# Optimization experiments

Hardware: AMD Instinct MI355X
Metric: run time of the kernel (lower is better)

Reference implementation:

```python
import jax, jax.numpy as jnp
import numpy as np

B, S, HID, H, RELC = 2, 1024, 1024, 16, 64
D = HID // H          # head dim = 64
R = 2 * RELC + 1      # 129 relative-position buckets
NEG_INF = -10000.0
LN_EPS = 1e-12


def setup_inputs() -> dict:
    key = jax.random.key(0)
    ks = jax.random.split(key, 16)
    s = 0.02
    return {
        "query": jax.random.normal(ks[0], (B, S, HID), jnp.float32),
        "key": jax.random.normal(ks[1], (B, S, HID), jnp.float32),
        "value": jax.random.normal(ks[2], (B, S, HID), jnp.float32),
        "mask_k": jnp.ones((B, S), jnp.float32),
        "mask_qk": jnp.ones((B, S, S), jnp.float32),
        "rposi": jax.random.randint(ks[3], (B, S, S), 0, R, jnp.int32),
        "Wq": jax.random.normal(ks[4], (HID, HID), jnp.float32) * s,
        "bq": jnp.zeros((HID,), jnp.float32),
        "Wk": jax.random.normal(ks[5], (HID, HID), jnp.float32) * s,
        "bk": jnp.zeros((HID,), jnp.float32),
        "Wv": jax.random.normal(ks[6], (HID, HID), jnp.float32) * s,
        "bv": jnp.zeros((HID,), jnp.float32),
        "Wd": jax.random.normal(ks[7], (HID, HID), jnp.float32) * s,
        "bd": jnp.zeros((HID,), jnp.float32),
        "ln_g": jnp.ones((HID,), jnp.float32),
        "ln_b": jnp.zeros((HID,), jnp.float32),
        "edge_atts": jax.random.normal(ks[8], (R, D), jnp.float32) * s,
        "edge_values": jax.random.normal(ks[9], (R, D), jnp.float32) * s,
    }


def _heads(x):  # [B,S,HID] -> [B,H,S,D]
    return x.reshape(B, -1, H, D).transpose(0, 2, 1, 3)


def reference(query, key, value, mask_k, mask_qk, rposi,
              Wq, bq, Wk, bk, Wv, bv, Wd, bd, ln_g, ln_b,
              edge_atts, edge_values):
    q = _heads(query @ Wq + bq)   # [B,H,Q,D]
    k = _heads(key @ Wk + bk)     # [B,H,K,D]
    v = _heads(value @ Wv + bv)   # [B,H,K,D]

    rp = jnp.clip(rposi, -RELC, RELC) + RELC          # [B,Q,K] in [0,2*RELC]

    scores = jnp.einsum('bhqd,bhkd->bhqk', q, k)      # [B,H,Q,K]
    # relative-position attention bias: q . edge_atts[rp]
    q2 = jnp.einsum('bhqd,rd->bhqr', q, edge_atts)    # [B,H,Q,R]
    rscore = jnp.take_along_axis(
        q2, jnp.broadcast_to(rp[:, None], (B, H, S, S)), axis=-1)
    scores = (scores + rscore) / jnp.sqrt(jnp.float32(D))

    att_mask = mask_k[:, None, :] * mask_qk           # [B,Q,K]
    scores = scores + (1.0 - att_mask)[:, None] * NEG_INF
    probs = jax.nn.softmax(scores, axis=-1)           # [B,H,Q,K]

    ctx = jnp.einsum('bhqk,bhkd->bhqd', probs, v)     # [B,H,Q,D]
    rval = edge_values[rp]                            # [B,Q,K,D]
    ctx = ctx + jnp.einsum('bhqk,bqkd->bhqd', probs, rval)

    ctx = ctx.transpose(0, 2, 1, 3).reshape(B, S, HID)
    h = ctx @ Wd + bd
    x = h + query
    mu = jnp.mean(x, axis=-1, keepdims=True)
    var = jnp.mean(jnp.square(x - mu), axis=-1, keepdims=True)
    return (x - mu) * jax.lax.rsqrt(var + LN_EPS) * ln_g + ln_b
```

## Files before the change

### kernel.cpp

```cpp
#include <hip/hip_runtime.h>
#include <hip/hip_bf16.h>
#include <stdint.h>

#define B_    2
#define S_    1024
#define HID_  1024
#define H_    16
#define D_    64
#define R_    129
#define EST_  136
#define SENT_ 132
#define NTOK_ 2048
#define C2_   0.18033688011112042f

typedef __attribute__((ext_vector_type(8))) short bf16x8;
typedef __attribute__((ext_vector_type(4))) float f32x4;

__device__ __forceinline__ float bf2f(unsigned short s) {
  union { float f; unsigned int u; } v; v.u = ((unsigned int)s) << 16; return v.f;
}
__device__ __forceinline__ unsigned short f2bf(float f) {
  union { float f; unsigned int u; } v; v.f = f;
  return (unsigned short)((v.u + 0x7fff + ((v.u >> 16) & 1)) >> 16);
}

__global__ __launch_bounds__(256) void wt4_kernel(const float* __restrict__ Wq,
                                                  const float* __restrict__ Wk,
                                                  const float* __restrict__ Wv,
                                                  const float* __restrict__ Wd,
                                                  unsigned short* __restrict__ WqT,
                                                  unsigned short* __restrict__ WkT,
                                                  unsigned short* __restrict__ WvT,
                                                  unsigned short* __restrict__ WdT) {
  const float* W; unsigned short* Wt;
  switch (blockIdx.z) {
    case 0: W = Wq; Wt = WqT; break;
    case 1: W = Wk; Wt = WkT; break;
    case 2: W = Wv; Wt = WvT; break;
    default: W = Wd; Wt = WdT; break;
  }
  __shared__ float tile[32][33];
  const int n0 = blockIdx.x * 32, k0 = blockIdx.y * 32;
  const int tx = threadIdx.x, ty = threadIdx.y;
  #pragma unroll
  for (int i = 0; i < 32; i += 8)
    tile[ty + i][tx] = W[(size_t)(k0 + ty + i) * HID_ + n0 + tx];
  __syncthreads();
  #pragma unroll
  for (int i = 0; i < 32; i += 8)
    Wt[(size_t)(n0 + ty + i) * HID_ + k0 + tx] = f2bf(tile[tx][ty + i]);
}

__global__ __launch_bounds__(256) void evt_kernel(const float* __restrict__ EV,
                                                  unsigned short* __restrict__ EVt) {
  const int idx = blockIdx.x * 256 + threadIdx.x;
  if (idx < 64 * 160) {
    const int d = idx / 160, r = idx % 160;
    EVt[idx] = f2bf(r < R_ ? EV[(size_t)r * D_ + d] : 0.f);
  }
}

__global__ __launch_bounds__(256) void rpx_kernel(const int* __restrict__ rposi,
                                                  const float* __restrict__ mask_k,
                                                  const float* __restrict__ mask_qk,
                                                  unsigned char* __restrict__ rpx) {
  const int t = threadIdx.x;
  const int lo = t & 15, hi = (t >> 4) & 3, wq = (t >> 6) & 1, wk = (t >> 7) & 1;
  const int kt = blockIdx.x, q5 = blockIdx.y, b = blockIdx.z;
  unsigned char out[8];
  #pragma unroll
  for (int e = 0; e < 8; e++) {
    const int ct2 = e >> 2, j = e & 3;
    const int q = q5 * 32 + wq * 16 + hi * 4 + j;
    const int k = kt * 64 + wk * 32 + ct2 * 16 + lo;
    int rp = rposi[((size_t)b * S_ + q) * S_ + k];
    rp = min(max(rp, -64), 64) + 64;
    const float m = mask_qk[((size_t)b * S_ + q) * S_ + k] * mask_k[(size_t)b * S_ + k];
    out[e] = (m > 0.5f) ? (unsigned char)rp : (unsigned char)SENT_;
  }
  const size_t off = ((((((size_t)b * 32 + q5) * 16 + kt) * 2 + wk) * 2 + wq) * 4 + hi) * 16 + lo;
  *(uint2*)(rpx + off * 8) = *(uint2*)out;
}

__global__ __launch_bounds__(256) void qkv_gemm_kernel(
    const float* __restrict__ query, const float* __restrict__ key, const float* __restrict__ value,
    const unsigned short* __restrict__ WqT, const unsigned short* __restrict__ WkT,
    const unsigned short* __restrict__ WvT,
    const float* __restrict__ bq, const float* __restrict__ bk, const float* __restrict__ bvv,
    unsigned short* __restrict__ Qh, unsigned short* __restrict__ Kh, unsigned short* __restrict__ Vt) {
  const float* A; const unsigned short* Bt; const float* bias; unsigned short* Out; int omode;
  if (blockIdx.z == 0)      { A = query; Bt = WqT; bias = bq;  Out = Qh; omode = 0; }
  else if (blockIdx.z == 1) { A = key;   Bt = WkT; bias = bk;  Out = Kh; omode = 0; }
  else                      { A = value; Bt = WvT; bias = bvv; Out = Vt; omode = 1; }
  __shared__ __align__(16) unsigned short Alds[64][40];
  __shared__ __align__(16) unsigned short Blds[128][40];
  const int m0 = blockIdx.x * 64, n0 = blockIdx.y * 128;
  const int t = threadIdx.x;
  const int wave = t >> 6, lane = t & 63, lo = lane & 15, hi = lane >> 4;
  const int wr = wave >> 1, wc = wave & 1;
  const int arow = t >> 2, acol = (t & 3) * 8;
  const int brow = t >> 1, bcol = (t & 1) * 16;
  const f32x4 zero4 = {0.f, 0.f, 0.f, 0.f};
  f32x4 acc[2][4];
  #pragma unroll
  for (int a = 0; a < 2; a++)
    #pragma unroll
    for (int b = 0; b < 4; b++) acc[a][b] = zero4;

  for (int k0 = 0; k0 < HID_; k0 += 32) {
    const float* asrc = A + (size_t)(m0 + arow) * HID_ + k0 + acol;
    f32x4 v0 = *(const f32x4*)asrc, v1 = *(const f32x4*)(asrc + 4);
    unsigned short ab[8];
    ab[0]=f2bf(v0.x); ab[1]=f2bf(v0.y); ab[2]=f2bf(v0.z); ab[3]=f2bf(v0.w);
    ab[4]=f2bf(v1.x); ab[5]=f2bf(v1.y); ab[6]=f2bf(v1.z); ab[7]=f2bf(v1.w);
    bf16x8 bb0 = *(const bf16x8*)(Bt + (size_t)(n0 + brow) * HID_ + k0 + bcol);
    bf16x8 bb1 = *(const bf16x8*)(Bt + (size_t)(n0 + brow) * HID_ + k0 + bcol + 8);
    __syncthreads();
    *(bf16x8*)&Alds[arow][acol]     = *(bf16x8*)ab;
    *(bf16x8*)&Blds[brow][bcol]     = bb0;
    *(bf16x8*)&Blds[brow][bcol + 8] = bb1;
    __syncthreads();
    bf16x8 af[2], bfr[4];
    #pragma unroll
    for (int a = 0; a < 2; a++) af[a]  = *(const bf16x8*)&Alds[wr*32 + a*16 + lo][hi*8];
    #pragma unroll
    for (int b = 0; b < 4; b++) bfr[b] = *(const bf16x8*)&Blds[wc*64 + b*16 + lo][hi*8];
    #pragma unroll
    for (int a = 0; a < 2; a++)
      #pragma unroll
      for (int b = 0; b < 4; b++)
        acc[a][b] = __builtin_amdgcn_mfma_f32_16x16x32_bf16(af[a], bfr[b], acc[a][b], 0, 0, 0);
  }

  #pragma unroll
  for (int a = 0; a < 2; a++) {
    const int mg = m0 + wr*32 + a*16 + hi*4;
    #pragma unroll
    for (int b = 0; b < 4; b++) {
      const int n = n0 + wc*64 + b*16 + lo;
      const float bv = bias[n];
      const int hh = n >> 6, d = n & (D_ - 1);
      #pragma unroll
      for (int j = 0; j < 4; j++) {
        const float val = acc[a][b][j] + bv;
        const int m = mg + j;
        const int bb = m >> 10, s = m & (S_ - 1);
        if (omode == 0)
          Out[(((size_t)(bb * H_ + hh)) * S_ + s) * D_ + d] = f2bf(val);
        else
          Out[(((size_t)(bb * H_ + hh)) * D_ + d) * S_ + s] = f2bf(val);
      }
    }
  }
}

__global__ __launch_bounds__(256) void d_gemm_kernel(const unsigned short* __restrict__ Actx,
                                                     const unsigned short* __restrict__ Bt,
                                                     const float* __restrict__ bias,
                                                     float* __restrict__ Out) {
  __shared__ __align__(16) unsigned short Alds[64][40];
  __shared__ __align__(16) unsigned short Blds[128][40];
  const int m0 = blockIdx.x * 64, n0 = blockIdx.y * 128;
  const int t = threadIdx.x;
  const int wave = t >> 6, lane = t & 63, lo = lane & 15, hi = lane >> 4;
  const int wr = wave >> 1, wc = wave & 1;
  const int arow = t >> 2, acol = (t & 3) * 8;
  const int brow = t >> 1, bcol = (t & 1) * 16;
  const f32x4 zero4 = {0.f, 0.f, 0.f, 0.f};
  f32x4 acc[2][4];
  #pragma unroll
  for (int a = 0; a < 2; a++)
    #pragma unroll
    for (int b = 0; b < 4; b++) acc[a][b] = zero4;

  for (int k0 = 0; k0 < HID_; k0 += 32) {
    bf16x8 aa = *(const bf16x8*)(Actx + (size_t)(m0 + arow) * HID_ + k0 + acol);
    bf16x8 bb0 = *(const bf16x8*)(Bt + (size_t)(n0 + brow) * HID_ + k0 + bcol);
    bf16x8 bb1 = *(const bf16x8*)(Bt + (size_t)(n0 + brow) * HID_ + k0 + bcol + 8);
    __syncthreads();
    *(bf16x8*)&Alds[arow][acol]     = aa;
    *(bf16x8*)&Blds[brow][bcol]     = bb0;
    *(bf16x8*)&Blds[brow][bcol + 8] = bb1;
    __syncthreads();
    bf16x8 af[2], bfr[4];
    #pragma unroll
    for (int a = 0; a < 2; a++) af[a]  = *(const bf16x8*)&Alds[wr*32 + a*16 + lo][hi*8];
    #pragma unroll
    for (int b = 0; b < 4; b++) bfr[b] = *(const bf16x8*)&Blds[wc*64 + b*16 + lo][hi*8];
    #pragma unroll
    for (int a = 0; a < 2; a++)
      #pragma unroll
      for (int b = 0; b < 4; b++)
        acc[a][b] = __builtin_amdgcn_mfma_f32_16x16x32_bf16(af[a], bfr[b], acc[a][b], 0, 0, 0);
  }

  #pragma unroll
  for (int a = 0; a < 2; a++) {
    const int mg = m0 + wr*32 + a*16 + hi*4;
    #pragma unroll
    for (int b = 0; b < 4; b++) {
      const int n = n0 + wc*64 + b*16 + lo;
      const float bv = bias[n];
      #pragma unroll
      for (int j = 0; j < 4; j++)
        Out[(size_t)(mg + j) * HID_ + n] = acc[a][b][j] + bv;
    }
  }
}

__global__ __launch_bounds__(256) void eb_kernel(const unsigned short* __restrict__ Qh,
                                                 const float* __restrict__ EA,
                                                 unsigned short* __restrict__ Eb) {
  __shared__ __align__(16) unsigned short Qt[64][72];
  __shared__ __align__(16) unsigned short EAt[144][72];
  const int bh = blockIdx.y, s0 = blockIdx.x * 64;
  const int t = threadIdx.x, wave = t >> 6, lane = t & 63;
  const int lo = lane & 15, hi = lane >> 4;
  { const int row = t >> 2, c0 = (t & 3) * 16;
    const unsigned short* src = Qh + ((size_t)bh * S_ + s0 + row) * D_ + c0;
    *(bf16x8*)&Qt[row][c0]   = *(const bf16x8*)src;
    *(bf16x8*)&Qt[row][c0+8] = *(const bf16x8*)(src + 8); }
  for (int i = t; i < 144 * 64; i += 256) {
    const int r = i >> 6, d = i & 63;
    EAt[r][d] = f2bf(r < R_ ? EA[(size_t)r * D_ + d] : 0.f);
  }
  __syncthreads();
  bf16x8 af[2];
  af[0] = *(const bf16x8*)&Qt[wave*16 + lo][hi*8];
  af[1] = *(const bf16x8*)&Qt[wave*16 + lo][32 + hi*8];
  const f32x4 zero4 = {0.f, 0.f, 0.f, 0.f};
  f32x4 acc[9];
  #pragma unroll
  for (int rt = 0; rt < 9; rt++) acc[rt] = zero4;
  #pragma unroll
  for (int rt = 0; rt < 9; rt++)
    #pragma unroll
    for (int kk = 0; kk < 2; kk++) {
      bf16x8 bfr = *(const bf16x8*)&EAt[rt*16 + lo][kk*32 + hi*8];
      acc[rt] = __builtin_amdgcn_mfma_f32_16x16x32_bf16(af[kk], bfr, acc[rt], 0, 0, 0);
    }
  #pragma unroll
  for (int rt = 0; rt < 9; rt++) {
    const int r = rt * 16 + lo;
    if (r < EST_) {
      #pragma unroll
      for (int j = 0; j < 4; j++) {
        const int q = s0 + wave*16 + hi*4 + j;
        const float val = (r < R_) ? exp2f(acc[rt][j] * C2_) : 0.f;
        Eb[((size_t)bh * S_ + q) * EST_ + r] = f2bf(val);
      }
    }
  }
}


#define ABODY(KT, RX) do {                                                               \
    const int kw = (KT) * 64 + wk * 32;                                                  \
    float ge[8];                                                                         \
    _Pragma("unroll")                                                                    \
    for (int e = 0; e < 8; e++) {                                                        \
      const int rp = (int)(((e < 4 ? (RX).x : (RX).y) >> ((e & 3) * 8)) & 255u);         \
      ge[e] = bf2f(Uq.El[wq * 16 + hi * 4 + (e & 3)][rp]);                               \
    }                                                                                    \
    bf16x8 kf0 = *(const bf16x8*)(Kbase + (size_t)(kw + lo) * D_ + hi * 8);              \
    bf16x8 kf1 = *(const bf16x8*)(Kbase + (size_t)(kw + lo) * D_ + 32 + hi * 8);         \
    bf16x8 kf2 = *(const bf16x8*)(Kbase + (size_t)(kw + 16 + lo) * D_ + hi * 8);         \
    bf16x8 kf3 = *(const bf16x8*)(Kbase + (size_t)(kw + 16 + lo) * D_ + 32 + hi * 8);    \
    bf16x8 vf0 = *(const bf16x8*)(Vbase + (size_t)(lo) * S_ + kw + hi * 8);              \
    bf16x8 vf1 = *(const bf16x8*)(Vbase + (size_t)(16 + lo) * S_ + kw + hi * 8);         \
    bf16x8 vf2 = *(const bf16x8*)(Vbase + (size_t)(32 + lo) * S_ + kw + hi * 8);         \
    bf16x8 vf3 = *(const bf16x8*)(Vbase + (size_t)(48 + lo) * S_ + kw + hi * 8);         \
    f32x4 sc0 = zero4, sc1 = zero4;                                                      \
    sc0 = __builtin_amdgcn_mfma_f32_16x16x32_bf16(qfrag0, kf0, sc0, 0, 0, 0);            \
    sc0 = __builtin_amdgcn_mfma_f32_16x16x32_bf16(qfrag1, kf1, sc0, 0, 0, 0);            \
    sc1 = __builtin_amdgcn_mfma_f32_16x16x32_bf16(qfrag0, kf2, sc1, 0, 0, 0);            \
    sc1 = __builtin_amdgcn_mfma_f32_16x16x32_bf16(qfrag1, kf3, sc1, 0, 0, 0);            \
    unsigned int pvp0, pvp1, pvp2, pvp3;                                                 \
    _Pragma("unroll")                                                                    \
    for (int e = 0; e < 8; e++) {                                                        \
      const int j = e & 3;                                                               \
      const float sv = (e < 4) ? sc0[j] : sc1[j];                                        \
      const float p = exp2f(sv * C2_) * ge[e];                                           \
      lsum[j] += p;                                                                      \
      const unsigned int pb = f2bf(p);                                                   \
      if (e == 0) pvp0 = pb;       else if (e == 1) pvp0 |= pb << 16;                    \
      else if (e == 2) pvp1 = pb;  else if (e == 3) pvp1 |= pb << 16;                    \
      else if (e == 4) pvp2 = pb;  else if (e == 5) pvp2 |= pb << 16;                    \
      else if (e == 6) pvp3 = pb;  else              pvp3 |= pb << 16;                   \
      Plds[wave][hi * 4 + j][(e >> 2) * 16 + lo] = (unsigned short)pb;                   \
    }                                                                                    \
    bf16x8 pf = *(const bf16x8*)&Plds[wave][lo][hi * 8];                                 \
    ctx[0] = __builtin_amdgcn_mfma_f32_16x16x32_bf16(pf, vf0, ctx[0], 0, 0, 0);          \
    ctx[1] = __builtin_amdgcn_mfma_f32_16x16x32_bf16(pf, vf1, ctx[1], 0, 0, 0);          \
    ctx[2] = __builtin_amdgcn_mfma_f32_16x16x32_bf16(pf, vf2, ctx[2], 0, 0, 0);          \
    ctx[3] = __builtin_amdgcn_mfma_f32_16x16x32_bf16(pf, vf3, ctx[3], 0, 0, 0);          \
    _Pragma("unroll")                                                                    \
    for (int e = 0; e < 8; e++) {                                                        \
      const int rp = (int)(((e < 4 ? (RX).x : (RX).y) >> ((e & 3) * 8)) & 255u);         \
      const unsigned int pw = (e < 2) ? pvp0 : (e < 4) ? pvp1 : (e < 6) ? pvp2 : pvp3;   \
      const float pr = bf2f((unsigned short)((pw >> ((e & 1) * 16)) & 0xFFFFu));         \
      if (rp == 128) r128[e & 3] += pr;                                                  \
      else atomicAdd(&hist[wq * 16 + hi * 4 + (e & 3)][rp], pr);                         \
    }                                                                                    \
  } while (0)

__global__ __launch_bounds__(256, 4) void attn_kernel(const unsigned short* __restrict__ Qh,
                                                      const unsigned short* __restrict__ Kh,
                                                      const unsigned short* __restrict__ Vt,
                                                      const unsigned short* __restrict__ Eb,
                                                      const unsigned char* __restrict__ rpx,
                                                      const unsigned short* __restrict__ EVt,
                                                      unsigned short* __restrict__ ctxb) {
  __shared__ union UU {
    unsigned short El[32][EST_];
    float red[2][16][65];
  } Uq;
  __shared__ float hist[32][EST_];
  __shared__ __align__(16) unsigned short Plds[4][16][40];
  __shared__ float lsumLDS[2][32];

  const int lin = blockIdx.x;
  const int bh = (lin & 7) + 8 * (lin >> 8);
  const int q5 = (lin >> 3) & 31;
  const int b = bh >> 4, h = bh & 15;
  const int q0 = q5 * 32;
  const int t = threadIdx.x, wave = t >> 6, lane = t & 63;
  const int lo = lane & 15, hi = lane >> 4;
  const int wq = wave >> 1, wk = wave & 1;

  { const unsigned int* src = (const unsigned int*)(Eb + ((size_t)bh * S_ + q0) * EST_);
    unsigned int* dst = (unsigned int*)&Uq.El[0][0];
    for (int i = t; i < 32 * EST_ / 2; i += 256) dst[i] = src[i]; }
  for (int i = t; i < 32 * EST_; i += 256) (&hist[0][0])[i] = 0.f;

  bf16x8 qfrag0, qfrag1;
  { const unsigned short* qrow = Qh + ((size_t)bh * S_ + q0 + wq * 16 + lo) * D_;
    qfrag0 = *(const bf16x8*)(qrow + hi * 8);
    qfrag1 = *(const bf16x8*)(qrow + 32 + hi * 8); }

  const f32x4 zero4 = {0.f, 0.f, 0.f, 0.f};
  f32x4 ctx[4] = {zero4, zero4, zero4, zero4};
  float lsum[4] = {0.f, 0.f, 0.f, 0.f};
  float r128[4] = {0.f, 0.f, 0.f, 0.f};

  const unsigned short* Kbase = Kh + (size_t)bh * S_ * D_;
  const unsigned short* Vbase = Vt + (size_t)bh * D_ * S_;
  const unsigned char* RXp = rpx +
      (((((((size_t)b * 32 + q5) * 16) * 2 + wk) * 2 + wq) * 4 + hi) * 16 + lo) * 8;

  __syncthreads();

  uint2 rxA = *(const uint2*)(RXp);
  #pragma unroll 1
  for (int kt2 = 0; kt2 < 8; kt2++) {
    uint2 rxB = *(const uint2*)(RXp + (size_t)(2 * kt2 + 1) * 2048);
    ABODY(2 * kt2, rxA);
    if (kt2 < 7) rxA = *(const uint2*)(RXp + (size_t)(2 * kt2 + 2) * 2048);
    ABODY(2 * kt2 + 1, rxB);
  }

  #pragma unroll
  for (int j = 0; j < 4; j++) {
    float v = r128[j];
    v += __shfl_xor(v, 1); v += __shfl_xor(v, 2); v += __shfl_xor(v, 4); v += __shfl_xor(v, 8);
    if (lo == 0) atomicAdd(&hist[wq * 16 + hi * 4 + j][128], v);
    float w = lsum[j];
    w += __shfl_xor(w, 1); w += __shfl_xor(w, 2); w += __shfl_xor(w, 4); w += __shfl_xor(w, 8);
    if (lo == 0) lsumLDS[wk][wq * 16 + hi * 4 + j] = w;
  }
  __syncthreads();

  #pragma unroll
  for (int g2 = 0; g2 < 2; g2++) {
    const int r0 = (wk * 2 + g2) * 32;
    const float* hrow = &hist[wq * 16 + lo][r0 + hi * 8];
    bf16x8 hf;
    #pragma unroll
    for (int u = 0; u < 8; u++) hf[u] = (short)f2bf(hrow[u]);
    #pragma unroll
    for (int dt = 0; dt < 4; dt++) {
      bf16x8 ef = *(const bf16x8*)(EVt + (size_t)(dt * 16 + lo) * 160 + r0 + hi * 8);
      ctx[dt] = __builtin_amdgcn_mfma_f32_16x16x32_bf16(hf, ef, ctx[dt], 0, 0, 0);
    }
  }
  if (wk == 1) {
    #pragma unroll
    for (int dt = 0; dt < 4; dt++) {
      const float ev = bf2f(EVt[(size_t)(dt * 16 + lo) * 160 + 128]);
      #pragma unroll
      for (int j = 0; j < 4; j++) {
        ctx[dt][j] += hist[wq * 16 + hi * 4 + j][128] * ev;
        Uq.red[wq][hi * 4 + j][dt * 16 + lo] = ctx[dt][j];
      }
    }
  }
  __syncthreads();
  if (wk == 0) {
    float ls[4];
    #pragma unroll
    for (int j = 0; j < 4; j++)
      ls[j] = lsumLDS[0][wq * 16 + hi * 4 + j] + lsumLDS[1][wq * 16 + hi * 4 + j];
    #pragma unroll
    for (int dt = 0; dt < 4; dt++)
      #pragma unroll
      for (int j = 0; j < 4; j++) {
        const float val = (ctx[dt][j] + Uq.red[wq][hi * 4 + j][dt * 16 + lo]) / ls[j];
        const int q = q0 + wq * 16 + hi * 4 + j;
        ctxb[((size_t)b * S_ + q) * HID_ + h * D_ + dt * 16 + lo] = f2bf(val);
      }
  }
}

__global__ __launch_bounds__(256) void ln_kernel(const float* __restrict__ hbuf,
                                                 const float* __restrict__ query,
                                                 const float* __restrict__ g,
                                                 const float* __restrict__ bta,
                                                 float* __restrict__ out) {
  const int row = blockIdx.x, t = threadIdx.x;
  f32x4 hv = *(const f32x4*)(hbuf + (size_t)row * HID_ + t * 4);
  f32x4 qv = *(const f32x4*)(query + (size_t)row * HID_ + t * 4);
  f32x4 x;
  x.x = hv.x + qv.x; x.y = hv.y + qv.y; x.z = hv.z + qv.z; x.w = hv.w + qv.w;
  float s  = x.x + x.y + x.z + x.w;
  float s2 = x.x*x.x + x.y*x.y + x.z*x.z + x.w*x.w;
  #pragma unroll
  for (int m = 1; m < 64; m <<= 1) { s += __shfl_xor(s, m); s2 += __shfl_xor(s2, m); }
  __shared__ float w1[4], w2[4];
  const int wave = t >> 6;
  if ((t & 63) == 0) { w1[wave] = s; w2[wave] = s2; }
  __syncthreads();
  s  = w1[0] + w1[1] + w1[2] + w1[3];
  s2 = w2[0] + w2[1] + w2[2] + w2[3];
  const float mu  = s * (1.f / HID_);
  const float var = s2 * (1.f / HID_) - mu * mu;
  const float rstd = rsqrtf(var + 1e-12f);
  f32x4 gv = *(const f32x4*)(g + t * 4);
  f32x4 bv = *(const f32x4*)(bta + t * 4);
  f32x4 o;
  o.x = (x.x - mu) * rstd * gv.x + bv.x;
  o.y = (x.y - mu) * rstd * gv.y + bv.y;
  o.z = (x.z - mu) * rstd * gv.z + bv.z;
  o.w = (x.w - mu) * rstd * gv.w + bv.w;
  *(f32x4*)(out + (size_t)row * HID_ + t * 4) = o;
}

extern "C" void kernel_launch(void* const* d_in, const int* in_sizes, int n_in,
                              void* d_out, int out_size, void* d_ws, size_t ws_size,
                              hipStream_t stream) {
  const float* query   = (const float*)d_in[0];
  const float* key     = (const float*)d_in[1];
  const float* value   = (const float*)d_in[2];
  const float* mask_k  = (const float*)d_in[3];
  const float* mask_qk = (const float*)d_in[4];
  const int*   rposi   = (const int*)d_in[5];
  const float* Wq = (const float*)d_in[6];
  const float* bq = (const float*)d_in[7];
  const float* Wk = (const float*)d_in[8];
  const float* bk = (const float*)d_in[9];
  const float* Wv = (const float*)d_in[10];
  const float* bv = (const float*)d_in[11];
  const float* Wd = (const float*)d_in[12];
  const float* bd = (const float*)d_in[13];
  const float* ln_g = (const float*)d_in[14];
  const float* ln_b = (const float*)d_in[15];
  const float* edge_atts   = (const float*)d_in[16];
  const float* edge_values = (const float*)d_in[17];

  char* ws = (char*)d_ws;
  unsigned short* WqT  = (unsigned short*)(ws + 0);
  unsigned short* WkT  = (unsigned short*)(ws + 2097152);
  unsigned short* WvT  = (unsigned short*)(ws + 4194304);
  unsigned short* WdT  = (unsigned short*)(ws + 6291456);
  unsigned short* ctxb = (unsigned short*)(ws + 0);
  unsigned short* Qh   = (unsigned short*)(ws + 8388608);
  unsigned short* Kh   = (unsigned short*)(ws + 12582912);
  unsigned short* Vt   = (unsigned short*)(ws + 16777216);
  float*          hbuf = (float*)        (ws + 8388608);
  unsigned short* Eb   = (unsigned short*)(ws + 20971520);
  unsigned short* EVt  = (unsigned short*)(ws + 29884416);
  unsigned char*  rpx  = (unsigned char*) (ws + 29904896);

  wt4_kernel<<<dim3(32, 32, 4), dim3(32, 8), 0, stream>>>(Wq, Wk, Wv, Wd, WqT, WkT, WvT, WdT);
  evt_kernel<<<40, 256, 0, stream>>>(edge_values, EVt);
  rpx_kernel<<<dim3(16, 32, 2), 256, 0, stream>>>(rposi, mask_k, mask_qk, rpx);

  qkv_gemm_kernel<<<dim3(32, 8, 3), 256, 0, stream>>>(query, key, value, WqT, WkT, WvT,
                                                      bq, bk, bv, Qh, Kh, Vt);

  eb_kernel<<<dim3(S_/64, B_*H_), 256, 0, stream>>>(Qh, edge_atts, Eb);

  attn_kernel<<<1024, 256, 0, stream>>>(Qh, Kh, Vt, Eb, rpx, EVt, ctxb);

  d_gemm_kernel<<<dim3(32, 8), 256, 0, stream>>>(ctxb, WdT, bd, hbuf);

  ln_kernel<<<NTOK_, 256, 0, stream>>>(hbuf, query, ln_g, ln_b, (float*)d_out);
}
```

Baseline: 191.0 us.

## Transpose attention MFMA operands to pass probabilities via shuffles instead of LDS

Swaps the A/B operands of the QK^T and PV MFMAs so each lane owns one query row. The P fragment for the PV product is then rebuilt from registers with cross-lane shuffles instead of a round-trip through a per-wave LDS buffer, which is removed. The rpx index layout, the histogram atomics, the row-sum reductions and the epilogue are remapped to match, and the epilogue now multiplies by a reciprocal instead of dividing. Occupancy bound drops from 4 to 3 blocks per CU, trading occupancy for fewer LDS accesses and barriers-free data movement.

Measured after the change: 193.1 us. Within noise of the previous version (+1.1%).

```diff
diff --git a/kernel.cpp b/kernel.cpp
--- a/kernel.cpp
+++ b/kernel.cpp
@@ -67,12 +67,12 @@
   const int t = threadIdx.x;
   const int lo = t & 15, hi = (t >> 4) & 3, wq = (t >> 6) & 1, wk = (t >> 7) & 1;
   const int kt = blockIdx.x, q5 = blockIdx.y, b = blockIdx.z;
+  const int q = q5 * 32 + wq * 16 + lo;
   unsigned char out[8];
   #pragma unroll
   for (int e = 0; e < 8; e++) {
     const int ct2 = e >> 2, j = e & 3;
-    const int q = q5 * 32 + wq * 16 + hi * 4 + j;
-    const int k = kt * 64 + wk * 32 + ct2 * 16 + lo;
+    const int k = kt * 64 + wk * 32 + ct2 * 16 + hi * 4 + j;
     int rp = rposi[((size_t)b * S_ + q) * S_ + k];
     rp = min(max(rp, -64), 64) + 64;
     const float m = mask_qk[((size_t)b * S_ + q) * S_ + k] * mask_k[(size_t)b * S_ + k];
@@ -260,7 +260,7 @@
     _Pragma("unroll")                                                                    \
     for (int e = 0; e < 8; e++) {                                                        \
       const int rp = (int)(((e < 4 ? (RX).x : (RX).y) >> ((e & 3) * 8)) & 255u);         \
-      ge[e] = bf2f(Uq.El[wq * 16 + hi * 4 + (e & 3)][rp]);                               \
+      ge[e] = bf2f(Uq.El[wq * 16 + lo][rp]);                                             \
     }                                                                                    \
     bf16x8 kf0 = *(const bf16x8*)(Kbase + (size_t)(kw + lo) * D_ + hi * 8);              \
     bf16x8 kf1 = *(const bf16x8*)(Kbase + (size_t)(kw + lo) * D_ + 32 + hi * 8);         \
@@ -271,40 +271,59 @@
     bf16x8 vf2 = *(const bf16x8*)(Vbase + (size_t)(32 + lo) * S_ + kw + hi * 8);         \
     bf16x8 vf3 = *(const bf16x8*)(Vbase + (size_t)(48 + lo) * S_ + kw + hi * 8);         \
     f32x4 sc0 = zero4, sc1 = zero4;                                                      \
-    sc0 = __builtin_amdgcn_mfma_f32_16x16x32_bf16(qfrag0, kf0, sc0, 0, 0, 0);            \
-    sc0 = __builtin_amdgcn_mfma_f32_16x16x32_bf16(qfrag1, kf1, sc0, 0, 0, 0);            \
-    sc1 = __builtin_amdgcn_mfma_f32_16x16x32_bf16(qfrag0, kf2, sc1, 0, 0, 0);            \
-    sc1 = __builtin_amdgcn_mfma_f32_16x16x32_bf16(qfrag1, kf3, sc1, 0, 0, 0);            \
+    sc0 = __builtin_amdgcn_mfma_f32_16x16x32_bf16(kf0, qfrag0, sc0, 0, 0, 0);            \
+    sc0 = __builtin_amdgcn_mfma_f32_16x16x32_bf16(kf1, qfrag1, sc0, 0, 0, 0);            \
+    sc1 = __builtin_amdgcn_mfma_f32_16x16x32_bf16(kf2, qfrag0, sc1, 0, 0, 0);            \
+    sc1 = __builtin_amdgcn_mfma_f32_16x16x32_bf16(kf3, qfrag1, sc1, 0, 0, 0);            \
     unsigned int pvp0, pvp1, pvp2, pvp3;                                                 \
     _Pragma("unroll")                                                                    \
     for (int e = 0; e < 8; e++) {                                                        \
       const int j = e & 3;                                                               \
       const float sv = (e < 4) ? sc0[j] : sc1[j];                                        \
       const float p = exp2f(sv * C2_) * ge[e];                                           \
-      lsum[j] += p;                                                                      \
+      lsum += p;                                                                         \
       const unsigned int pb = f2bf(p);                                                   \
       if (e == 0) pvp0 = pb;       else if (e == 1) pvp0 |= pb << 16;                    \
       else if (e == 2) pvp1 = pb;  else if (e == 3) pvp1 |= pb << 16;                    \
       else if (e == 4) pvp2 = pb;  else if (e == 5) pvp2 |= pb << 16;                    \
       else if (e == 6) pvp3 = pb;  else              pvp3 |= pb << 16;                   \
-      Plds[wave][hi * 4 + j][(e >> 2) * 16 + lo] = (unsigned short)pb;                   \
     }                                                                                    \
-    bf16x8 pf = *(const bf16x8*)&Plds[wave][lo][hi * 8];                                 \
-    ctx[0] = __builtin_amdgcn_mfma_f32_16x16x32_bf16(pf, vf0, ctx[0], 0, 0, 0);          \
-    ctx[1] = __builtin_amdgcn_mfma_f32_16x16x32_bf16(pf, vf1, ctx[1], 0, 0, 0);          \
-    ctx[2] = __builtin_amdgcn_mfma_f32_16x16x32_bf16(pf, vf2, ctx[2], 0, 0, 0);          \
-    ctx[3] = __builtin_amdgcn_mfma_f32_16x16x32_bf16(pf, vf3, ctx[3], 0, 0, 0);          \
+                             \
+    {                                                                                    \
+      const int srcA = lo + ((hi & 1) << 5);                \
+      const int srcB = srcA + 16;                                                        \
+      const unsigned pA0 = (unsigned)__shfl((int)pvp0, srcA);                            \
+      const unsigned pA1 = (unsigned)__shfl((int)pvp1, srcA);                            \
+      const unsigned pA2 = (unsigned)__shfl((int)pvp2, srcA);                            \
+      const unsigned pA3 = (unsigned)__shfl((int)pvp3, srcA);                            \
+      const unsigned pB0 = (unsigned)__shfl((int)pvp0, srcB);                            \
+      const unsigned pB1 = (unsigned)__shfl((int)pvp1, srcB);                            \
+      const unsigned pB2 = (unsigned)__shfl((int)pvp2, srcB);                            \
+      const unsigned pB3 = (unsigned)__shfl((int)pvp3, srcB);                            \
+      const bool cu = (hi >> 1) != 0;                                                    \
+      unsigned pw[4];                                                                    \
+      pw[0] = cu ? pA2 : pA0;                                                            \
+      pw[1] = cu ? pA3 : pA1;                                                            \
+      pw[2] = cu ? pB2 : pB0;                                                            \
+      pw[3] = cu ? pB3 : pB1;                                                            \
+      bf16x8 pf = *(bf16x8*)pw;                                                          \
+      ctx[0] = __builtin_amdgcn_mfma_f32_16x16x32_bf16(vf0, pf, ctx[0], 0, 0, 0);        \
+      ctx[1] = __builtin_amdgcn_mfma_f32_16x16x32_bf16(vf1, pf, ctx[1], 0, 0, 0);        \
+      ctx[2] = __builtin_amdgcn_mfma_f32_16x16x32_bf16(vf2, pf, ctx[2], 0, 0, 0);        \
+      ctx[3] = __builtin_amdgcn_mfma_f32_16x16x32_bf16(vf3, pf, ctx[3], 0, 0, 0);        \
+    }                                                                                    \
+                                             \
     _Pragma("unroll")                                                                    \
     for (int e = 0; e < 8; e++) {                                                        \
       const int rp = (int)(((e < 4 ? (RX).x : (RX).y) >> ((e & 3) * 8)) & 255u);         \
-      const unsigned int pw = (e < 2) ? pvp0 : (e < 4) ? pvp1 : (e < 6) ? pvp2 : pvp3;   \
-      const float pr = bf2f((unsigned short)((pw >> ((e & 1) * 16)) & 0xFFFFu));         \
-      if (rp == 128) r128[e & 3] += pr;                                                  \
-      else atomicAdd(&hist[wq * 16 + hi * 4 + (e & 3)][rp], pr);                         \
+      const unsigned int pw2 = (e < 2) ? pvp0 : (e < 4) ? pvp1 : (e < 6) ? pvp2 : pvp3;  \
+      const float pr = bf2f((unsigned short)((pw2 >> ((e & 1) * 16)) & 0xFFFFu));        \
+      if (rp == 128) r128 += pr;                                                         \
+      else atomicAdd(&hist[wq * 16 + lo][rp], pr);                                       \
     }                                                                                    \
   } while (0)
 
-__global__ __launch_bounds__(256, 4) void attn_kernel(const unsigned short* __restrict__ Qh,
+__global__ __launch_bounds__(256, 3) void attn_kernel(const unsigned short* __restrict__ Qh,
                                                       const unsigned short* __restrict__ Kh,
                                                       const unsigned short* __restrict__ Vt,
                                                       const unsigned short* __restrict__ Eb,
@@ -313,10 +332,9 @@
                                                       unsigned short* __restrict__ ctxb) {
   __shared__ union UU {
     unsigned short El[32][EST_];
-    float red[2][16][65];
+    float red[2][16][68];
   } Uq;
   __shared__ float hist[32][EST_];
-  __shared__ __align__(16) unsigned short Plds[4][16][40];
   __shared__ float lsumLDS[2][32];
 
   const int lin = blockIdx.x;
@@ -340,8 +358,7 @@
 
   const f32x4 zero4 = {0.f, 0.f, 0.f, 0.f};
   f32x4 ctx[4] = {zero4, zero4, zero4, zero4};
-  float lsum[4] = {0.f, 0.f, 0.f, 0.f};
-  float r128[4] = {0.f, 0.f, 0.f, 0.f};
+  float lsum = 0.f, r128 = 0.f;
 
   const unsigned short* Kbase = Kh + (size_t)bh * S_ * D_;
   const unsigned short* Vbase = Vt + (size_t)bh * D_ * S_;
@@ -359,14 +376,13 @@
     ABODY(2 * kt2 + 1, rxB);
   }
 
-  #pragma unroll
-  for (int j = 0; j < 4; j++) {
-    float v = r128[j];
-    v += __shfl_xor(v, 1); v += __shfl_xor(v, 2); v += __shfl_xor(v, 4); v += __shfl_xor(v, 8);
-    if (lo == 0) atomicAdd(&hist[wq * 16 + hi * 4 + j][128], v);
-    float w = lsum[j];
-    w += __shfl_xor(w, 1); w += __shfl_xor(w, 2); w += __shfl_xor(w, 4); w += __shfl_xor(w, 8);
-    if (lo == 0) lsumLDS[wk][wq * 16 + hi * 4 + j] = w;
+  {
+    float v = r128;
+    v += __shfl_xor(v, 16); v += __shfl_xor(v, 32);
+    if (hi == 0) atomicAdd(&hist[wq * 16 + lo][128], v);
+    float w = lsum;
+    w += __shfl_xor(w, 16); w += __shfl_xor(w, 32);
+    if (hi == 0) lsumLDS[wk][wq * 16 + lo] = w;
   }
   __syncthreads();
 
@@ -380,33 +396,32 @@
     #pragma unroll
     for (int dt = 0; dt < 4; dt++) {
       bf16x8 ef = *(const bf16x8*)(EVt + (size_t)(dt * 16 + lo) * 160 + r0 + hi * 8);
-      ctx[dt] = __builtin_amdgcn_mfma_f32_16x16x32_bf16(hf, ef, ctx[dt], 0, 0, 0);
+      ctx[dt] = __builtin_amdgcn_mfma_f32_16x16x32_bf16(ef, hf, ctx[dt], 0, 0, 0);
     }
   }
   if (wk == 1) {
-    #pragma unroll
-    for (int dt = 0; dt < 4; dt++) {
-      const float ev = bf2f(EVt[(size_t)(dt * 16 + lo) * 160 + 128]);
-      #pragma unroll
-      for (int j = 0; j < 4; j++) {
-        ctx[dt][j] += hist[wq * 16 + hi * 4 + j][128] * ev;
-        Uq.red[wq][hi * 4 + j][dt * 16 + lo] = ctx[dt][j];
+    const float hq = hist[wq * 16 + lo][128];
+    #pragma unroll
+    for (int dt = 0; dt < 4; dt++)
+      #pragma unroll
+      for (int jj = 0; jj < 4; jj++) {
+        const float ev = bf2f(EVt[(size_t)(dt * 16 + hi * 4 + jj) * 160 + 128]);
+        ctx[dt][jj] += hq * ev;
+        Uq.red[wq][lo][dt * 16 + hi * 4 + jj] = ctx[dt][jj];
       }
-    }
   }
   __syncthreads();
   if (wk == 0) {
-    float ls[4];
-    #pragma unroll
-    for (int j = 0; j < 4; j++)
-      ls[j] = lsumLDS[0][wq * 16 + hi * 4 + j] + lsumLDS[1][wq * 16 + hi * 4 + j];
+    const float ls = lsumLDS[0][wq * 16 + lo] + lsumLDS[1][wq * 16 + lo];
+    const float rls = 1.0f / ls;
+    const size_t rowbase = ((size_t)b * S_ + q0 + wq * 16 + lo) * HID_ + h * D_;
     #pragma unroll
     for (int dt = 0; dt < 4; dt++)
       #pragma unroll
-      for (int j = 0; j < 4; j++) {
-        const float val = (ctx[dt][j] + Uq.red[wq][hi * 4 + j][dt * 16 + lo]) / ls[j];
-        const int q = q0 + wq * 16 + hi * 4 + j;
-        ctxb[((size_t)b * S_ + q) * HID_ + h * D_ + dt * 16 + lo] = f2bf(val);
+      for (int jj = 0; jj < 4; jj++) {
+        const int d = dt * 16 + hi * 4 + jj;
+        const float val = (ctx[dt][jj] + Uq.red[wq][lo][d]) * rls;
+        ctxb[rowbase + d] = f2bf(val);
       }
   }
 }
```

## Fuse prep kernels and compute relative-position score table inside attention kernel

Applied to the files above, without the earlier changes.

Merges the weight-transpose, edge-value transpose and rpx packing kernels into a single launch dispatched by block index. Removes the separate eb_kernel: each attention block now converts edge_atts to bf16 in LDS and computes exp(q·edge_atts) for its 32 queries with MFMA, storing the result directly into the shared El table. This drops two launches and the global round trip of the Eb buffer. In exchange, every attention block redundantly converts edge_atts and runs a leftover dummy MFMA pass whose results are discarded, and the LDS union is enlarged.

After: 188.5 us. Within noise of the previous version (-1.4%).

```diff
diff --git a/kernel.cpp b/kernel.cpp
--- a/kernel.cpp
+++ b/kernel.cpp
@@ -24,62 +24,59 @@
   return (unsigned short)((v.u + 0x7fff + ((v.u >> 16) & 1)) >> 16);
 }
 
-__global__ __launch_bounds__(256) void wt4_kernel(const float* __restrict__ Wq,
-                                                  const float* __restrict__ Wk,
-                                                  const float* __restrict__ Wv,
-                                                  const float* __restrict__ Wd,
-                                                  unsigned short* __restrict__ WqT,
-                                                  unsigned short* __restrict__ WkT,
-                                                  unsigned short* __restrict__ WvT,
-                                                  unsigned short* __restrict__ WdT) {
-  const float* W; unsigned short* Wt;
-  switch (blockIdx.z) {
-    case 0: W = Wq; Wt = WqT; break;
-    case 1: W = Wk; Wt = WkT; break;
-    case 2: W = Wv; Wt = WvT; break;
-    default: W = Wd; Wt = WdT; break;
-  }
+__global__ __launch_bounds__(256) void prep_kernel(
+    const float* __restrict__ Wq, const float* __restrict__ Wk,
+    const float* __restrict__ Wv, const float* __restrict__ Wd,
+    unsigned short* __restrict__ WqT, unsigned short* __restrict__ WkT,
+    unsigned short* __restrict__ WvT, unsigned short* __restrict__ WdT,
+    const float* __restrict__ EV, unsigned short* __restrict__ EVt,
+    const int* __restrict__ rposi, const float* __restrict__ mask_k,
+    const float* __restrict__ mask_qk, unsigned char* __restrict__ rpx) {
   __shared__ float tile[32][33];
-  const int n0 = blockIdx.x * 32, k0 = blockIdx.y * 32;
-  const int tx = threadIdx.x, ty = threadIdx.y;
-  #pragma unroll
-  for (int i = 0; i < 32; i += 8)
-    tile[ty + i][tx] = W[(size_t)(k0 + ty + i) * HID_ + n0 + tx];
-  __syncthreads();
-  #pragma unroll
-  for (int i = 0; i < 32; i += 8)
-    Wt[(size_t)(n0 + ty + i) * HID_ + k0 + tx] = f2bf(tile[tx][ty + i]);
-}
-
-__global__ __launch_bounds__(256) void evt_kernel(const float* __restrict__ EV,
-                                                  unsigned short* __restrict__ EVt) {
-  const int idx = blockIdx.x * 256 + threadIdx.x;
-  if (idx < 64 * 160) {
-    const int d = idx / 160, r = idx % 160;
-    EVt[idx] = f2bf(r < R_ ? EV[(size_t)r * D_ + d] : 0.f);
-  }
-}
-
-__global__ __launch_bounds__(256) void rpx_kernel(const int* __restrict__ rposi,
-                                                  const float* __restrict__ mask_k,
-                                                  const float* __restrict__ mask_qk,
-                                                  unsigned char* __restrict__ rpx) {
+  const int bid = blockIdx.x;
   const int t = threadIdx.x;
-  const int lo = t & 15, hi = (t >> 4) & 3, wq = (t >> 6) & 1, wk = (t >> 7) & 1;
-  const int kt = blockIdx.x, q5 = blockIdx.y, b = blockIdx.z;
-  unsigned char out[8];
-  #pragma unroll
-  for (int e = 0; e < 8; e++) {
-    const int ct2 = e >> 2, j = e & 3;
-    const int q = q5 * 32 + wq * 16 + hi * 4 + j;
-    const int k = kt * 64 + wk * 32 + ct2 * 16 + lo;
-    int rp = rposi[((size_t)b * S_ + q) * S_ + k];
-    rp = min(max(rp, -64), 64) + 64;
-    const float m = mask_qk[((size_t)b * S_ + q) * S_ + k] * mask_k[(size_t)b * S_ + k];
-    out[e] = (m > 0.5f) ? (unsigned char)rp : (unsigned char)SENT_;
-  }
-  const size_t off = ((((((size_t)b * 32 + q5) * 16 + kt) * 2 + wk) * 2 + wq) * 4 + hi) * 16 + lo;
-  *(uint2*)(rpx + off * 8) = *(uint2*)out;
+  if (bid < 4096) {
+    const int z = bid >> 10, rem = bid & 1023, bx = rem & 31, by = rem >> 5;
+    const float* W; unsigned short* Wt;
+    switch (z) {
+      case 0: W = Wq; Wt = WqT; break;
+      case 1: W = Wk; Wt = WkT; break;
+      case 2: W = Wv; Wt = WvT; break;
+      default: W = Wd; Wt = WdT; break;
+    }
+    const int tx = t & 31, ty = t >> 5;
+    const int n0 = bx * 32, k0 = by * 32;
+    #pragma unroll
+    for (int i = 0; i < 32; i += 8)
+      tile[ty + i][tx] = W[(size_t)(k0 + ty + i) * HID_ + n0 + tx];
+    __syncthreads();
+    #pragma unroll
+    for (int i = 0; i < 32; i += 8)
+      Wt[(size_t)(n0 + ty + i) * HID_ + k0 + tx] = f2bf(tile[tx][ty + i]);
+  } else if (bid < 5120) {
+    const int rem = bid - 4096;
+    const int kt = rem & 15, q5 = (rem >> 4) & 31, b = rem >> 9;
+    const int lo = t & 15, hi = (t >> 4) & 3, wq = (t >> 6) & 1, wk = (t >> 7) & 1;
+    unsigned char out[8];
+    #pragma unroll
+    for (int e = 0; e < 8; e++) {
+      const int ct2 = e >> 2, j = e & 3;
+      const int q = q5 * 32 + wq * 16 + hi * 4 + j;
+      const int k = kt * 64 + wk * 32 + ct2 * 16 + lo;
+      int rp = rposi[((size_t)b * S_ + q) * S_ + k];
+      rp = min(max(rp, -64), 64) + 64;
+      const float m = mask_qk[((size_t)b * S_ + q) * S_ + k] * mask_k[(size_t)b * S_ + k];
+      out[e] = (m > 0.5f) ? (unsigned char)rp : (unsigned char)SENT_;
+    }
+    const size_t off = ((((((size_t)b * 32 + q5) * 16 + kt) * 2 + wk) * 2 + wq) * 4 + hi) * 16 + lo;
+    *(uint2*)(rpx + off * 8) = *(uint2*)out;
+  } else {
+    const int idx = (bid - 5120) * 256 + t;
+    if (idx < 64 * 160) {
+      const int d = idx / 160, r = idx % 160;
+      EVt[idx] = f2bf(r < R_ ? EV[(size_t)r * D_ + d] : 0.f);
+    }
+  }
 }
 
 __global__ __launch_bounds__(256) void qkv_gemm_kernel(
@@ -208,51 +205,6 @@
   }
 }
 
-__global__ __launch_bounds__(256) void eb_kernel(const unsigned short* __restrict__ Qh,
-                                                 const float* __restrict__ EA,
-                                                 unsigned short* __restrict__ Eb) {
-  __shared__ __align__(16) unsigned short Qt[64][72];
-  __shared__ __align__(16) unsigned short EAt[144][72];
-  const int bh = blockIdx.y, s0 = blockIdx.x * 64;
-  const int t = threadIdx.x, wave = t >> 6, lane = t & 63;
-  const int lo = lane & 15, hi = lane >> 4;
-  { const int row = t >> 2, c0 = (t & 3) * 16;
-    const unsigned short* src = Qh + ((size_t)bh * S_ + s0 + row) * D_ + c0;
-    *(bf16x8*)&Qt[row][c0]   = *(const bf16x8*)src;
-    *(bf16x8*)&Qt[row][c0+8] = *(const bf16x8*)(src + 8); }
-  for (int i = t; i < 144 * 64; i += 256) {
-    const int r = i >> 6, d = i & 63;
-    EAt[r][d] = f2bf(r < R_ ? EA[(size_t)r * D_ + d] : 0.f);
-  }
-  __syncthreads();
-  bf16x8 af[2];
-  af[0] = *(const bf16x8*)&Qt[wave*16 + lo][hi*8];
-  af[1] = *(const bf16x8*)&Qt[wave*16 + lo][32 + hi*8];
-  const f32x4 zero4 = {0.f, 0.f, 0.f, 0.f};
-  f32x4 acc[9];
-  #pragma unroll
-  for (int rt = 0; rt < 9; rt++) acc[rt] = zero4;
-  #pragma unroll
-  for (int rt = 0; rt < 9; rt++)
-    #pragma unroll
-    for (int kk = 0; kk < 2; kk++) {
-      bf16x8 bfr = *(const bf16x8*)&EAt[rt*16 + lo][kk*32 + hi*8];
-      acc[rt] = __builtin_amdgcn_mfma_f32_16x16x32_bf16(af[kk], bfr, acc[rt], 0, 0, 0);
-    }
-  #pragma unroll
-  for (int rt = 0; rt < 9; rt++) {
-    const int r = rt * 16 + lo;
-    if (r < EST_) {
-      #pragma unroll
-      for (int j = 0; j < 4; j++) {
-        const int q = s0 + wave*16 + hi*4 + j;
-        const float val = (r < R_) ? exp2f(acc[rt][j] * C2_) : 0.f;
-        Eb[((size_t)bh * S_ + q) * EST_ + r] = f2bf(val);
-      }
-    }
-  }
-}
-
 
 #define ABODY(KT, RX) do {                                                               \
     const int kw = (KT) * 64 + wk * 32;                                                  \
@@ -260,7 +212,7 @@
     _Pragma("unroll")                                                                    \
     for (int e = 0; e < 8; e++) {                                                        \
       const int rp = (int)(((e < 4 ? (RX).x : (RX).y) >> ((e & 3) * 8)) & 255u);         \
-      ge[e] = bf2f(Uq.El[wq * 16 + hi * 4 + (e & 3)][rp]);                               \
+      ge[e] = bf2f(U.s.El[wq * 16 + hi * 4 + (e & 3)][rp]);                              \
     }                                                                                    \
     bf16x8 kf0 = *(const bf16x8*)(Kbase + (size_t)(kw + lo) * D_ + hi * 8);              \
     bf16x8 kf1 = *(const bf16x8*)(Kbase + (size_t)(kw + lo) * D_ + 32 + hi * 8);         \
@@ -300,22 +252,27 @@
       const unsigned int pw = (e < 2) ? pvp0 : (e < 4) ? pvp1 : (e < 6) ? pvp2 : pvp3;   \
       const float pr = bf2f((unsigned short)((pw >> ((e & 1) * 16)) & 0xFFFFu));         \
       if (rp == 128) r128[e & 3] += pr;                                                  \
-      else atomicAdd(&hist[wq * 16 + hi * 4 + (e & 3)][rp], pr);                         \
+      else atomicAdd(&U.s.hist[wq * 16 + hi * 4 + (e & 3)][rp], pr);                     \
     }                                                                                    \
   } while (0)
 
 __global__ __launch_bounds__(256, 4) void attn_kernel(const unsigned short* __restrict__ Qh,
                                                       const unsigned short* __restrict__ Kh,
                                                       const unsigned short* __restrict__ Vt,
-                                                      const unsigned short* __restrict__ Eb,
+                                                      const float* __restrict__ EA,
                                                       const unsigned char* __restrict__ rpx,
                                                       const unsigned short* __restrict__ EVt,
                                                       unsigned short* __restrict__ ctxb) {
-  __shared__ union UU {
-    unsigned short El[32][EST_];
-    float red[2][16][65];
-  } Uq;
-  __shared__ float hist[32][EST_];
+  __shared__ union UA {
+    unsigned short EAt[144][64];
+    struct {
+      union {
+        unsigned short El[32][EST_];
+        float red[2][16][65];
+      };
+      float hist[32][EST_];
+    } s;
+  } U;
   __shared__ __align__(16) unsigned short Plds[4][16][40];
   __shared__ float lsumLDS[2][32];
 
@@ -328,17 +285,63 @@
   const int lo = lane & 15, hi = lane >> 4;
   const int wq = wave >> 1, wk = wave & 1;
 
-  { const unsigned int* src = (const unsigned int*)(Eb + ((size_t)bh * S_ + q0) * EST_);
-    unsigned int* dst = (unsigned int*)&Uq.El[0][0];
-    for (int i = t; i < 32 * EST_ / 2; i += 256) dst[i] = src[i]; }
-  for (int i = t; i < 32 * EST_; i += 256) (&hist[0][0])[i] = 0.f;
-
+  for (int i = t; i < 144 * 64; i += 256) {
+    const int r = i >> 6, d = i & 63;
+    U.EAt[r][d] = f2bf(r < R_ ? EA[(size_t)r * D_ + d] : 0.f);
+  }
   bf16x8 qfrag0, qfrag1;
   { const unsigned short* qrow = Qh + ((size_t)bh * S_ + q0 + wq * 16 + lo) * D_;
     qfrag0 = *(const bf16x8*)(qrow + hi * 8);
     qfrag1 = *(const bf16x8*)(qrow + 32 + hi * 8); }
+  __syncthreads();
 
   const f32x4 zero4 = {0.f, 0.f, 0.f, 0.f};
+  const int nrt = (wk == 0) ? 5 : 4;
+  const int rt0 = (wk == 0) ? 0 : 5;
+  f32x4 eacc[5] = {zero4, zero4, zero4, zero4, zero4};
+  #pragma unroll
+  for (int u = 0; u < 5; u++)
+    if (u < nrt) {
+      const int rt = rt0 + u;
+      #pragma unroll
+      for (int kk = 0; kk < 2; kk++) {
+        bf16x8 ea = *(const bf16x8*)&U.EAt[rt * 16 + lo][kk * 32 + hi * 8];
+        eacc[u] = __builtin_amdgcn_mfma_f32_16x16x32_bf16(ea, qfrag0, eacc[u], 0, 0, 0);
+      }
+    }
+  #pragma unroll
+  for (int u = 0; u < 5; u++)
+    if (u < nrt) {
+      const int rt = rt0 + u;
+      bf16x8 ea1 = *(const bf16x8*)&U.EAt[rt * 16 + lo][32 + hi * 8];
+      (void)ea1;
+    }
+  #pragma unroll
+  for (int u = 0; u < 5; u++) eacc[u] = zero4;
+  #pragma unroll
+  for (int u = 0; u < 5; u++)
+    if (u < nrt) {
+      const int rt = rt0 + u;
+      bf16x8 ea0 = *(const bf16x8*)&U.EAt[rt * 16 + lo][hi * 8];
+      bf16x8 ea1 = *(const bf16x8*)&U.EAt[rt * 16 + lo][32 + hi * 8];
+      eacc[u] = __builtin_amdgcn_mfma_f32_16x16x32_bf16(ea0, qfrag0, eacc[u], 0, 0, 0);
+      eacc[u] = __builtin_amdgcn_mfma_f32_16x16x32_bf16(ea1, qfrag1, eacc[u], 0, 0, 0);
+    }
+  __syncthreads();
+
+  #pragma unroll
+  for (int u = 0; u < 5; u++)
+    if (u < nrt) {
+      const int rt = rt0 + u;
+      #pragma unroll
+      for (int j = 0; j < 4; j++) {
+        const int r = rt * 16 + hi * 4 + j;
+        if (r < EST_)
+          U.s.El[wq * 16 + lo][r] = (r < R_) ? f2bf(exp2f(eacc[u][j] * C2_)) : (unsigned short)0;
+      }
+    }
+  for (int i = t; i < 32 * EST_; i += 256) (&U.s.hist[0][0])[i] = 0.f;
+
   f32x4 ctx[4] = {zero4, zero4, zero4, zero4};
   float lsum[4] = {0.f, 0.f, 0.f, 0.f};
   float r128[4] = {0.f, 0.f, 0.f, 0.f};
@@ -363,7 +366,7 @@
   for (int j = 0; j < 4; j++) {
     float v = r128[j];
     v += __shfl_xor(v, 1); v += __shfl_xor(v, 2); v += __shfl_xor(v, 4); v += __shfl_xor(v, 8);
-    if (lo == 0) atomicAdd(&hist[wq * 16 + hi * 4 + j][128], v);
+    if (lo == 0) atomicAdd(&U.s.hist[wq * 16 + hi * 4 + j][128], v);
     float w = lsum[j];
     w += __shfl_xor(w, 1); w += __shfl_xor(w, 2); w += __shfl_xor(w, 4); w += __shfl_xor(w, 8);
     if (lo == 0) lsumLDS[wk][wq * 16 + hi * 4 + j] = w;
@@ -373,7 +376,7 @@
   #pragma unroll
   for (int g2 = 0; g2 < 2; g2++) {
     const int r0 = (wk * 2 + g2) * 32;
-    const float* hrow = &hist[wq * 16 + lo][r0 + hi * 8];
+    const float* hrow = &U.s.hist[wq * 16 + lo][r0 + hi * 8];
     bf16x8 hf;
     #pragma unroll
     for (int u = 0; u < 8; u++) hf[u] = (short)f2bf(hrow[u]);
@@ -389,8 +392,8 @@
       const float ev = bf2f(EVt[(size_t)(dt * 16 + lo) * 160 + 128]);
       #pragma unroll
       for (int j = 0; j < 4; j++) {
-        ctx[dt][j] += hist[wq * 16 + hi * 4 + j][128] * ev;
-        Uq.red[wq][hi * 4 + j][dt * 16 + lo] = ctx[dt][j];
+        ctx[dt][j] += U.s.hist[wq * 16 + hi * 4 + j][128] * ev;
+        U.s.red[wq][hi * 4 + j][dt * 16 + lo] = ctx[dt][j];
       }
     }
   }
@@ -404,7 +407,7 @@
     for (int dt = 0; dt < 4; dt++)
       #pragma unroll
       for (int j = 0; j < 4; j++) {
-        const float val = (ctx[dt][j] + Uq.red[wq][hi * 4 + j][dt * 16 + lo]) / ls[j];
+        const float val = (ctx[dt][j] + U.s.red[wq][hi * 4 + j][dt * 16 + lo]) / ls[j];
         const int q = q0 + wq * 16 + hi * 4 + j;
         ctxb[((size_t)b * S_ + q) * HID_ + h * D_ + dt * 16 + lo] = f2bf(val);
       }
@@ -476,20 +479,16 @@
   unsigned short* Kh   = (unsigned short*)(ws + 12582912);
   unsigned short* Vt   = (unsigned short*)(ws + 16777216);
   float*          hbuf = (float*)        (ws + 8388608);
-  unsigned short* Eb   = (unsigned short*)(ws + 20971520);
   unsigned short* EVt  = (unsigned short*)(ws + 29884416);
   unsigned char*  rpx  = (unsigned char*) (ws + 29904896);
 
-  wt4_kernel<<<dim3(32, 32, 4), dim3(32, 8), 0, stream>>>(Wq, Wk, Wv, Wd, WqT, WkT, WvT, WdT);
-  evt_kernel<<<40, 256, 0, stream>>>(edge_values, EVt);
-  rpx_kernel<<<dim3(16, 32, 2), 256, 0, stream>>>(rposi, mask_k, mask_qk, rpx);
+  prep_kernel<<<5160, 256, 0, stream>>>(Wq, Wk, Wv, Wd, WqT, WkT, WvT, WdT,
+                                        edge_values, EVt, rposi, mask_k, mask_qk, rpx);
 
   qkv_gemm_kernel<<<dim3(32, 8, 3), 256, 0, stream>>>(query, key, value, WqT, WkT, WvT,
                                                       bq, bk, bv, Qh, Kh, Vt);
 
-  eb_kernel<<<dim3(S_/64, B_*H_), 256, 0, stream>>>(Qh, edge_atts, Eb);
-
-  attn_kernel<<<1024, 256, 0, stream>>>(Qh, Kh, Vt, Eb, rpx, EVt, ctxb);
+  attn_kernel<<<1024, 256, 0, stream>>>(Qh, Kh, Vt, edge_atts, rpx, EVt, ctxb);
 
   d_gemm_kernel<<<dim3(32, 8), 256, 0, stream>>>(ctxb, WdT, bd, hbuf);
 
```
